# Performance work log

Hardware: AMD Instinct MI355X
Metric: run time of the kernel (lower is better)

The kernel has to match this reference:

```python
import jax, jax.numpy as jnp
import numpy as np
from jax import lax

B = 16384
N_NUM = 32
N_CAT = 16
D = 256
D_HID = 512
N_LAYERS = 8
VOCAB = 100001  # total_cats + 1
OUT_DIM = 2
TOT_FEAT = N_NUM + N_CAT
EPS = 1e-5


def _layernorm(x, g, b):
    mu = jnp.mean(x, axis=-1, keepdims=True)
    var = jnp.mean(jnp.square(x - mu), axis=-1, keepdims=True)
    return (x - mu) * lax.rsqrt(var + EPS) * g + b


def setup_inputs() -> dict:
    key = jax.random.key(0)
    ks = jax.random.split(key, 16)
    s = 0.02
    return {
        "x_numerical": jax.random.normal(ks[0], (B, N_NUM, 1), dtype=jnp.float32),
        "x_categorical_idx": jax.random.randint(ks[1], (B, N_CAT), 0, VOCAB - 1, dtype=jnp.int32),
        # per-feature Linear(1, D): weight [N_NUM, D], bias [N_NUM, D]
        "w_num": jax.random.normal(ks[2], (N_NUM, D), dtype=jnp.float32) * s,
        "b_num": jnp.zeros((N_NUM, D), dtype=jnp.float32),
        "cat_embed": jax.random.normal(ks[3], (VOCAB, D), dtype=jnp.float32) * s,
        "W_first": jax.random.normal(ks[4], (TOT_FEAT * D, D), dtype=jnp.float32) * s,
        "b_first": jnp.zeros((D,), dtype=jnp.float32),
        # stacked block params, leading dim = N_LAYERS
        "ln_g": jnp.ones((N_LAYERS, D), dtype=jnp.float32),
        "ln_b": jnp.zeros((N_LAYERS, D), dtype=jnp.float32),
        "W1s": jax.random.normal(ks[5], (N_LAYERS, D, D_HID), dtype=jnp.float32) * s,
        "b1s": jnp.zeros((N_LAYERS, D_HID), dtype=jnp.float32),
        "W2s": jax.random.normal(ks[6], (N_LAYERS, D_HID, D), dtype=jnp.float32) * s,
        "b2s": jnp.zeros((N_LAYERS, D), dtype=jnp.float32),
        "g_f": jnp.ones((D,), dtype=jnp.float32),
        "beta_f": jnp.zeros((D,), dtype=jnp.float32),
        "W_head": jax.random.normal(ks[7], (D, OUT_DIM), dtype=jnp.float32) * s,
        "b_head": jnp.zeros((OUT_DIM,), dtype=jnp.float32),
    }


def reference(x_numerical, x_categorical_idx, w_num, b_num, cat_embed,
              W_first, b_first, ln_g, ln_b, W1s, b1s, W2s, b2s,
              g_f, beta_f, W_head, b_head):
    # numerical embeddings: per-feature Linear(1, D), vectorized over features
    x_val = x_numerical[:, :, 0:1]                       # [B, N_NUM, 1]
    x_n_emb = x_val * w_num[None] + b_num[None]          # [B, N_NUM, D]
    x_c_emb = cat_embed[x_categorical_idx]               # [B, N_CAT, D]
    x = jnp.concatenate([x_n_emb, x_c_emb], axis=1)      # [B, TOT_FEAT, D]
    x = x.reshape(x.shape[0], -1)                        # [B, TOT_FEAT*D]
    x = x @ W_first + b_first                            # [B, D]

    def block(h, params):
        g, bn, W1, b1, W2, b2 = params
        out = _layernorm(h, g, bn)
        out = jax.nn.relu(out @ W1 + b1)                 # dropout = identity (eval)
        out = out @ W2 + b2
        return h + out, None

    x, _ = lax.scan(block, x, (ln_g, ln_b, W1s, b1s, W2s, b2s))
    x = _layernorm(x, g_f, beta_f)
    logits = x @ W_head + b_head                         # [B, OUT_DIM]
    return logits
```

## Files before the change

### kernel.cpp

```cpp
#include <hip/hip_runtime.h>

typedef unsigned short u16;
typedef unsigned int u32;
typedef __attribute__((ext_vector_type(8))) short bf16x8;
typedef __attribute__((ext_vector_type(4))) float f32x4;

#define LDK 72

__device__ __forceinline__ u16 f2bf(float f) {
    u32 u = __float_as_uint(f);
    u += 0x7fffu + ((u >> 16) & 1u);
    return (u16)(u >> 16);
}

__device__ __forceinline__ f32x4 mfma16(bf16x8 a, bf16x8 b, f32x4 c) {
    return __builtin_amdgcn_mfma_f32_16x16x32_bf16(a, b, c, 0, 0, 0);
}


__global__ __launch_bounds__(256) void prep_u_kernel(
    const float* __restrict__ w_num, const float* __restrict__ b_num,
    const float* __restrict__ W_first, float* __restrict__ Upart, float* __restrict__ Ppart)
{
    __shared__ float wrow[32];
    __shared__ float brow[32];
    int j = threadIdx.x, f = blockIdx.x, ks = blockIdx.y;
    if (j < 32) {
        wrow[j] = w_num[f * 256 + ks * 32 + j];
        brow[j] = b_num[f * 256 + ks * 32 + j];
    }
    __syncthreads();
    float au = 0.f, ap = 0.f;
#pragma unroll 8
    for (int k = 0; k < 32; k++) {
        float w = W_first[(size_t)((f << 8) + ks * 32 + k) * 256 + j];
        au = fmaf(wrow[k], w, au);
        ap = fmaf(brow[k], w, ap);
    }
    Upart[(size_t)(ks * 32 + f) * 256 + j] = au;
    Ppart[(size_t)(ks * 32 + f) * 256 + j] = ap;
}

__global__ __launch_bounds__(256) void prep_reduce_kernel(
    const float* __restrict__ Upart, const float* __restrict__ Ppart,
    float* __restrict__ U, float* __restrict__ P)
{
    int j = threadIdx.x, f = blockIdx.x;
    float au = 0.f, ap = 0.f;
#pragma unroll
    for (int ks = 0; ks < 8; ks++) {
        au += Upart[(size_t)(ks * 32 + f) * 256 + j];
        ap += Ppart[(size_t)(ks * 32 + f) * 256 + j];
    }
    U[f * 256 + j] = au;
    P[f * 256 + j] = ap;
}

__global__ __launch_bounds__(256) void prep_c0_kernel(
    const float* __restrict__ b_first, const float* __restrict__ P, float* __restrict__ c0)
{
    int j = threadIdx.x;
    float a = b_first[j];
#pragma unroll 8
    for (int f = 0; f < 32; f++) a += P[f * 256 + j];
    c0[j] = a;
}

__global__ __launch_bounds__(256) void transpose_kernel(
    const float* __restrict__ in, u16* __restrict__ out,
    int R, int C, int ldo, int k_off, size_t in_stride, size_t out_stride)
{
    __shared__ float t[64][65];
    in  += (size_t)blockIdx.z * in_stride;
    out += (size_t)blockIdx.z * out_stride;
    const int tid = threadIdx.x;
    const int r0 = blockIdx.x * 64, c0 = blockIdx.y * 64;
#pragma unroll
    for (int i = 0; i < 16; i++) {
        int e = tid + i * 256;
        int r = e >> 6, c = e & 63;
        float v = (r0 + r < R) ? in[(size_t)(r0 + r) * C + c0 + c] : 0.f;
        t[c][r] = v;
    }
    __syncthreads();
#pragma unroll
    for (int i = 0; i < 2; i++) {
        int e = tid + i * 256;
        int c = e >> 3, r8 = (e & 7) * 8;
        u16 tmp[8];
#pragma unroll
        for (int x = 0; x < 8; x++) tmp[x] = f2bf(t[c][r8 + x]);
        *(bf16x8*)&out[(size_t)(c0 + c) * ldo + k_off + r0 + r8] = *(bf16x8*)tmp;
    }
}

#define FBM 64

#define GATHER(KQ, G0, G1)                                                    \
    {                                                                         \
        int chunk = tid;                                                      \
        int r = chunk >> 4, c4 = chunk & 15;                                  \
        int k = (KQ) + c4 * 4;                                                \
        int rowi = (k < 4096) ? sidx[r * 16 + ((k >> 8) & 15)] : 0;           \
        G0 = *(const float4*)&cemb[(size_t)rowi * 256 + (k & 255)];           \
        if (k >= 4096) {                                                      \
            if (k < 4128) {                                                   \
                int c = r * 32 + (k - 4096);                                  \
                G0.x = sx[c]; G0.y = sx[c + 1];                               \
                G0.z = sx[c + 2]; G0.w = sx[c + 3];                           \
            } else G0 = make_float4(0.f, 0.f, 0.f, 0.f);                      \
        }                                                                     \
        chunk = tid + 512;                                                    \
        r = chunk >> 4; c4 = chunk & 15;                                      \
        k = (KQ) + c4 * 4;                                                    \
        rowi = (k < 4096) ? sidx[r * 16 + ((k >> 8) & 15)] : 0;               \
        G1 = *(const float4*)&cemb[(size_t)rowi * 256 + (k & 255)];           \
        if (k >= 4096) {                                                      \
            if (k < 4128) {                                                   \
                int c = r * 32 + (k - 4096);                                  \
                G1.x = sx[c]; G1.y = sx[c + 1];                               \
                G1.z = sx[c + 2]; G1.w = sx[c + 3];                           \
            } else G1 = make_float4(0.f, 0.f, 0.f, 0.f);                      \
        }                                                                     \
    }

#define WRITE_A(BUF, G0, G1)                                                  \
    {                                                                         \
        int chunk = tid;                                                      \
        int r = chunk >> 4, c4 = chunk & 15;                                  \
        ushort4 o;                                                            \
        o.x = f2bf(G0.x); o.y = f2bf(G0.y); o.z = f2bf(G0.z); o.w = f2bf(G0.w); \
        *(ushort4*)&Ab[BUF][r * LDK + c4 * 4] = o;                            \
        chunk = tid + 512;                                                    \
        r = chunk >> 4; c4 = chunk & 15;                                      \
        o.x = f2bf(G1.x); o.y = f2bf(G1.y); o.z = f2bf(G1.z); o.w = f2bf(G1.w); \
        *(ushort4*)&Ab[BUF][r * LDK + c4 * 4] = o;                            \
    }

#define DMA_B(BUF, KQ)                                                        \
    _Pragma("unroll")                                                         \
    for (int it = 0; it < 4; it++) {                                          \
        int chunk = it * 512 + tid;                                           \
        int r = chunk >> 3;                                                   \
        int c8 = (chunk & 7) ^ (r & 7);                                       \
        const u16* src = &BT[(size_t)r * 4160 + (KQ) + c8 * 8];               \
        __builtin_amdgcn_global_load_lds(                                     \
            (const __attribute__((address_space(1))) void*)src,               \
            (__attribute__((address_space(3))) void*)&Bb[BUF][(it * 512 + wv * 64) * 8], \
            16, 0, 0);                                                        \
    }

#define COMPUTE(AB, BB)                                                       \
    _Pragma("unroll")                                                         \
    for (int kk = 0; kk < 64; kk += 32) {                                     \
        bf16x8 af[2], bfr[4];                                                 \
        _Pragma("unroll")                                                     \
        for (int i = 0; i < 2; i++)                                           \
            af[i] = *(const bf16x8*)&Ab[AB][(wm * 32 + i * 16 + l16) * LDK + kk + quad * 8]; \
        _Pragma("unroll")                                                     \
        for (int j = 0; j < 4; j++) {                                         \
            int row = wn * 64 + j * 16 + l16;                                 \
            int c8L = quad + (kk >> 3);                                       \
            bfr[j] = *(const bf16x8*)&Bb[BB][row * 64 + ((c8L ^ (row & 7)) * 8)]; \
        }                                                                     \
        _Pragma("unroll")                                                     \
        for (int i = 0; i < 2; i++)                                           \
            _Pragma("unroll")                                                 \
            for (int j = 0; j < 4; j++)                                       \
                acc[i][j] = mfma16(af[i], bfr[j], acc[i][j]);                 \
    }

#define ITER(S, KQ, G0, G1)                                                   \
    {                                                                         \
        WRITE_A((S + 1) & 1, G0, G1);                                         \
        int kq2 = (KQ) + 128; if (kq2 > 4096) kq2 = 4096;                     \
        DMA_B((S + 2) & 3, kq2);                                              \
        __builtin_amdgcn_sched_barrier(0);                                    \
        GATHER((KQ) + 192, G0, G1);                                           \
        __builtin_amdgcn_sched_barrier(0);                                    \
        COMPUTE(S & 1, S);                                                    \
        asm volatile("s_waitcnt vmcnt(8) lgkmcnt(0)" ::: "memory");           \
        __builtin_amdgcn_s_barrier();                                         \
        __builtin_amdgcn_sched_barrier(0);                                    \
    }

__global__ __launch_bounds__(512, 2) void first_gemm_kernel(
    const u16* __restrict__ BT, const float* __restrict__ bias,
    float* __restrict__ outF,
    const int* __restrict__ cidx, const float* __restrict__ cemb,
    const float* __restrict__ xnum)
{
    __shared__ __align__(16) u16 Ab[2][FBM * LDK];
    __shared__ __align__(16) u16 Bb[4][256 * 64];
    __shared__ int   sidx[FBM * 16];
    __shared__ float sx[FBM * 32];

    const int tid  = threadIdx.x;
    const int lane = tid & 63;
    const int wv   = tid >> 6;
    const int wm   = wv >> 2;
    const int wn   = wv & 3;
    const int quad = lane >> 4;
    const int l16  = lane & 15;
    const int m0   = blockIdx.x * FBM;

    sidx[tid]       = cidx[m0 * 16 + tid];
    sidx[tid + 512] = cidx[m0 * 16 + tid + 512];
    {
        float4 v = *(const float4*)&xnum[(size_t)m0 * 32 + tid * 4];
        *(float4*)&sx[tid * 4] = v;
    }
    __syncthreads();

    f32x4 acc[2][4];
#pragma unroll
    for (int i = 0; i < 2; i++)
#pragma unroll
        for (int j = 0; j < 4; j++) acc[i][j] = (f32x4){0.f, 0.f, 0.f, 0.f};

    float4 ga0, ga1, pa0, pa1, pb0, pb1;

    GATHER(0, ga0, ga1);
    WRITE_A(0, ga0, ga1);
    DMA_B(0, 0);
    __builtin_amdgcn_sched_barrier(0);
    GATHER(64, pa0, pa1);
    __builtin_amdgcn_sched_barrier(0);
    DMA_B(1, 64);
    __builtin_amdgcn_sched_barrier(0);
    GATHER(128, pb0, pb1);
    __builtin_amdgcn_sched_barrier(0);
    asm volatile("s_waitcnt vmcnt(8) lgkmcnt(0)" ::: "memory");
    __builtin_amdgcn_s_barrier();
    __builtin_amdgcn_sched_barrier(0);

#pragma unroll 1
    for (int k0 = 0; k0 < 4096; k0 += 256) {
        ITER(0, k0 +   0, pa0, pa1);
        ITER(1, k0 +  64, pb0, pb1);
        ITER(2, k0 + 128, pa0, pa1);
        ITER(3, k0 + 192, pb0, pb1);
    }
    COMPUTE(0, 0);

#pragma unroll
    for (int i = 0; i < 2; i++) {
#pragma unroll
        for (int j = 0; j < 4; j++) {
            int col = wn * 64 + j * 16 + l16;
            float bs = bias[col];
#pragma unroll
            for (int r = 0; r < 4; r++) {
                int row = m0 + wm * 32 + i * 16 + quad * 4 + r;
                outF[(size_t)row * 256 + col] = acc[i][j][r] + bs;
            }
        }
    }
}

#define BAR()                                                                 \
    asm volatile("s_waitcnt lgkmcnt(0)" ::: "memory");                        \
    __builtin_amdgcn_s_barrier();                                             \
    __builtin_amdgcn_sched_barrier(0);

__global__ __launch_bounds__(512, 2) void stack_kernel(
    const float* __restrict__ h,
    const float* __restrict__ ln_g, const float* __restrict__ ln_b,
    const u16* __restrict__ W1T, const float* __restrict__ b1s,
    const u16* __restrict__ W2T, const float* __restrict__ b2s,
    const float* __restrict__ g_f, const float* __restrict__ beta_f,
    const float* __restrict__ Wh, const float* __restrict__ bh,
    float* __restrict__ out)
{
    __shared__ __align__(16) float hbuf[64 * 260];
    __shared__ __align__(16) u16   scratch[64 * 512];
    const int tid  = threadIdx.x;
    const int lane = tid & 63;
    const int wv   = tid >> 6;
    const int quad = lane >> 4;
    const int l16  = lane & 15;
    const int m0   = blockIdx.x * 64;

#pragma unroll
    for (int rr = 0; rr < 8; rr++) {
        int row = rr * 8 + wv;
        *(float4*)&hbuf[row * 260 + lane * 4] =
            *(const float4*)&h[(size_t)(m0 + row) * 256 + lane * 4];
    }
    BAR();

#pragma unroll 1
    for (int l = 0; l < 8; l++) {
        const u16* W1 = W1T + l * 131072;
        const u16* W2 = W2T + l * 131072;
        const float* bb1 = b1s + l * 512;
        const float* bb2 = b2s + l * 256;

        float4 gv4 = *(const float4*)&ln_g[l * 256 + lane * 4];
        float4 bv4 = *(const float4*)&ln_b[l * 256 + lane * 4];
#pragma unroll
        for (int rr = 0; rr < 8; rr++) {
            int row = rr * 8 + wv;
            float4 x = *(const float4*)&hbuf[row * 260 + lane * 4];
            float s  = x.x + x.y + x.z + x.w;
            float s2 = x.x * x.x + x.y * x.y + x.z * x.z + x.w * x.w;
#pragma unroll
            for (int o = 32; o > 0; o >>= 1) { s += __shfl_xor(s, o); s2 += __shfl_xor(s2, o); }
            float mu = s * (1.f / 256.f);
            float rs = rsqrtf(s2 * (1.f / 256.f) - mu * mu + 1e-5f);
            ushort4 o4;
            o4.x = f2bf((x.x - mu) * rs * gv4.x + bv4.x);
            o4.y = f2bf((x.y - mu) * rs * gv4.y + bv4.y);
            o4.z = f2bf((x.z - mu) * rs * gv4.z + bv4.z);
            o4.w = f2bf((x.w - mu) * rs * gv4.w + bv4.w);
            *(ushort4*)&scratch[row * 256 + (((lane >> 1) ^ (row & 7)) << 3) + (lane & 1) * 4] = o4;
        }
        BAR();

        float b1v[4];
#pragma unroll
        for (int j = 0; j < 4; j++) b1v[j] = bb1[wv * 64 + j * 16 + l16];
        f32x4 acc1[4][4];
#pragma unroll
        for (int i = 0; i < 4; i++)
#pragma unroll
            for (int j = 0; j < 4; j++) acc1[i][j] = (f32x4){0.f, 0.f, 0.f, 0.f};
#pragma unroll
        for (int ks = 0; ks < 8; ks++) {
            bf16x8 af[4], bw[4];
#pragma unroll
            for (int i = 0; i < 4; i++)
                af[i] = *(const bf16x8*)&scratch[(i * 16 + l16) * 256 +
                            (((ks * 4 + quad) ^ (l16 & 7)) << 3)];
#pragma unroll
            for (int j = 0; j < 4; j++)
                bw[j] = *(const bf16x8*)&W1[(size_t)(wv * 64 + j * 16 + l16) * 256 + ks * 32 + quad * 8];
#pragma unroll
            for (int i = 0; i < 4; i++)
#pragma unroll
                for (int j = 0; j < 4; j++)
                    acc1[i][j] = mfma16(af[i], bw[j], acc1[i][j]);
        }
        BAR();

#pragma unroll
        for (int i = 0; i < 4; i++)
#pragma unroll
            for (int j = 0; j < 4; j++)
#pragma unroll
                for (int r = 0; r < 4; r++) {
                    float v = acc1[i][j][r] + b1v[j];
                    v = v > 0.f ? v : 0.f;
                    int row2 = i * 16 + quad * 4 + r;
                    int col  = wv * 64 + j * 16 + l16;
                    scratch[row2 * 512 + (((col >> 3) ^ (row2 & 7)) << 3) + (col & 7)] = f2bf(v);
                }
        BAR();

        float b2v[2];
#pragma unroll
        for (int j = 0; j < 2; j++) b2v[j] = bb2[wv * 32 + j * 16 + l16];
        f32x4 acc2[4][2];
#pragma unroll
        for (int i = 0; i < 4; i++)
#pragma unroll
            for (int j = 0; j < 2; j++) acc2[i][j] = (f32x4){0.f, 0.f, 0.f, 0.f};
#pragma unroll
        for (int ks = 0; ks < 16; ks++) {
            bf16x8 af[4], bw[2];
#pragma unroll
            for (int i = 0; i < 4; i++)
                af[i] = *(const bf16x8*)&scratch[(i * 16 + l16) * 512 +
                            (((ks * 4 + quad) ^ (l16 & 7)) << 3)];
#pragma unroll
            for (int j = 0; j < 2; j++)
                bw[j] = *(const bf16x8*)&W2[(size_t)(wv * 32 + j * 16 + l16) * 512 + ks * 32 + quad * 8];
#pragma unroll
            for (int i = 0; i < 4; i++)
#pragma unroll
                for (int j = 0; j < 2; j++)
                    acc2[i][j] = mfma16(af[i], bw[j], acc2[i][j]);
        }

#pragma unroll
        for (int i = 0; i < 4; i++)
#pragma unroll
            for (int j = 0; j < 2; j++) {
                int col = wv * 32 + j * 16 + l16;
#pragma unroll
                for (int r = 0; r < 4; r++)
                    hbuf[(i * 16 + quad * 4 + r) * 260 + col] += acc2[i][j][r] + b2v[j];
            }
        BAR();
    }

    {
        float4 gv4 = *(const float4*)&g_f[lane * 4];
        float4 bv4 = *(const float4*)&beta_f[lane * 4];
        float4 wa = *(const float4*)&Wh[lane * 8];
        float4 wb = *(const float4*)&Wh[lane * 8 + 4];
        float bh0 = bh[0], bh1 = bh[1];
#pragma unroll
        for (int rr = 0; rr < 8; rr++) {
            int row = rr * 8 + wv;
            float4 x = *(const float4*)&hbuf[row * 260 + lane * 4];
            float s = x.x + x.y + x.z + x.w;
            float s2 = x.x * x.x + x.y * x.y + x.z * x.z + x.w * x.w;
#pragma unroll
            for (int o = 32; o > 0; o >>= 1) { s += __shfl_xor(s, o); s2 += __shfl_xor(s2, o); }
            float mu = s * (1.f / 256.f);
            float rs = rsqrtf(s2 * (1.f / 256.f) - mu * mu + 1e-5f);
            float xn0 = (x.x - mu) * rs * gv4.x + bv4.x;
            float xn1 = (x.y - mu) * rs * gv4.y + bv4.y;
            float xn2 = (x.z - mu) * rs * gv4.z + bv4.z;
            float xn3 = (x.w - mu) * rs * gv4.w + bv4.w;
            float d0 = xn0 * wa.x + xn1 * wa.z + xn2 * wb.x + xn3 * wb.z;
            float d1 = xn0 * wa.y + xn1 * wa.w + xn2 * wb.y + xn3 * wb.w;
#pragma unroll
            for (int o = 32; o > 0; o >>= 1) { d0 += __shfl_xor(d0, o); d1 += __shfl_xor(d1, o); }
            if (lane == 0) {
                out[(size_t)(m0 + row) * 2 + 0] = d0 + bh0;
                out[(size_t)(m0 + row) * 2 + 1] = d1 + bh1;
            }
        }
    }
}

extern "C" void kernel_launch(void* const* d_in, const int* in_sizes, int n_in,
                              void* d_out, int out_size, void* d_ws, size_t ws_size,
                              hipStream_t stream)
{
    const float* x_num   = (const float*)d_in[0];
    const int*   cidx    = (const int*)d_in[1];
    const float* w_num   = (const float*)d_in[2];
    const float* b_num   = (const float*)d_in[3];
    const float* cemb    = (const float*)d_in[4];
    const float* W_first = (const float*)d_in[5];
    const float* b_first = (const float*)d_in[6];
    const float* ln_g    = (const float*)d_in[7];
    const float* ln_b    = (const float*)d_in[8];
    const float* W1s     = (const float*)d_in[9];
    const float* b1s     = (const float*)d_in[10];
    const float* W2s     = (const float*)d_in[11];
    const float* b2s     = (const float*)d_in[12];
    const float* g_f     = (const float*)d_in[13];
    const float* beta_f  = (const float*)d_in[14];
    const float* W_head  = (const float*)d_in[15];
    const float* b_head  = (const float*)d_in[16];
    float* out = (float*)d_out;

    char* ws = (char*)d_ws;
    float* U   = (float*)(ws + 0);
    float* c0  = (float*)(ws + 32768);
    float* P   = (float*)(ws + 33792);
    u16* WcT   = (u16*)(ws + 66560);
    u16* W1T   = (u16*)(ws + 2196480);
    u16* W2T   = (u16*)(ws + 4293632);
    float* h   = (float*)(ws + 6390784);
    float* Upart = (float*)(ws + 2196480);
    float* Ppart = (float*)(ws + 2458624);

    prep_u_kernel<<<dim3(32, 8), 256, 0, stream>>>(w_num, b_num, W_first, Upart, Ppart);
    prep_reduce_kernel<<<32, 256, 0, stream>>>(Upart, Ppart, U, P);
    prep_c0_kernel<<<1, 256, 0, stream>>>(b_first, P, c0);
    transpose_kernel<<<dim3(64, 4, 1), 256, 0, stream>>>(
        W_first + (size_t)8192 * 256, WcT, 4096, 256, 4160, 0, 0, 0);
    transpose_kernel<<<dim3(1, 4, 1), 256, 0, stream>>>(
        U, WcT, 32, 256, 4160, 4096, 0, 0);
    transpose_kernel<<<dim3(4, 8, 8), 256, 0, stream>>>(
        W1s, W1T, 256, 512, 256, 0, 131072, 131072);
    transpose_kernel<<<dim3(8, 4, 8), 256, 0, stream>>>(
        W2s, W2T, 512, 256, 512, 0, 131072, 131072);

    first_gemm_kernel<<<256, 512, 0, stream>>>(
        WcT, c0, h, cidx, cemb, x_num);

    stack_kernel<<<256, 512, 0, stream>>>(
        h, ln_g, ln_b, W1T, b1s, W2T, b2s,
        g_f, beta_f, W_head, b_head, out);
}
```

Measured before the change: 463.7 us.

## Retile residual stack to 32-row blocks and fold bias reduction into first GEMM

The MLP stack kernel now processes 32 rows per block with 4 waves (512 blocks of 256 threads) instead of 64 rows with 8 waves. Each wave now covers more output columns, and LDS uses padded strides in place of the XOR swizzle. The separate c0 bias-reduction kernel is removed, and its sum over P is computed inside the first GEMM epilogue. This is meant to raise block count and parallelism and to drop one launch. The cost is that each weight tile is reused across half as many rows, so global weight traffic per row doubles, and padded LDS may bring bank conflicts.

```diff
diff --git a/kernel.cpp b/kernel.cpp
--- a/kernel.cpp
+++ b/kernel.cpp
@@ -54,16 +54,6 @@
     }
     U[f * 256 + j] = au;
     P[f * 256 + j] = ap;
-}
-
-__global__ __launch_bounds__(256) void prep_c0_kernel(
-    const float* __restrict__ b_first, const float* __restrict__ P, float* __restrict__ c0)
-{
-    int j = threadIdx.x;
-    float a = b_first[j];
-#pragma unroll 8
-    for (int f = 0; f < 32; f++) a += P[f * 256 + j];
-    c0[j] = a;
 }
 
 __global__ __launch_bounds__(256) void transpose_kernel(
@@ -185,7 +175,8 @@
     }
 
 __global__ __launch_bounds__(512, 2) void first_gemm_kernel(
-    const u16* __restrict__ BT, const float* __restrict__ bias,
+    const u16* __restrict__ BT, const float* __restrict__ bfirst,
+    const float* __restrict__ Pm,
     float* __restrict__ outF,
     const int* __restrict__ cidx, const float* __restrict__ cemb,
     const float* __restrict__ xnum)
@@ -243,27 +234,30 @@
     }
     COMPUTE(0, 0);
 
+    float bsv[4];
+#pragma unroll
+    for (int j = 0; j < 4; j++) {
+        int col = wn * 64 + j * 16 + l16;
+        float bs = bfirst[col];
+#pragma unroll 8
+        for (int f = 0; f < 32; f++) bs += Pm[f * 256 + col];
+        bsv[j] = bs;
+    }
 #pragma unroll
     for (int i = 0; i < 2; i++) {
 #pragma unroll
         for (int j = 0; j < 4; j++) {
             int col = wn * 64 + j * 16 + l16;
-            float bs = bias[col];
 #pragma unroll
             for (int r = 0; r < 4; r++) {
                 int row = m0 + wm * 32 + i * 16 + quad * 4 + r;
-                outF[(size_t)row * 256 + col] = acc[i][j][r] + bs;
+                outF[(size_t)row * 256 + col] = acc[i][j][r] + bsv[j];
             }
         }
     }
 }
 
-#define BAR()                                                                 \
-    asm volatile("s_waitcnt lgkmcnt(0)" ::: "memory");                        \
-    __builtin_amdgcn_s_barrier();                                             \
-    __builtin_amdgcn_sched_barrier(0);
-
-__global__ __launch_bounds__(512, 2) void stack_kernel(
+__global__ __launch_bounds__(256, 2) void stack_kernel(
     const float* __restrict__ h,
     const float* __restrict__ ln_g, const float* __restrict__ ln_b,
     const u16* __restrict__ W1T, const float* __restrict__ b1s,
@@ -272,22 +266,22 @@
     const float* __restrict__ Wh, const float* __restrict__ bh,
     float* __restrict__ out)
 {
-    __shared__ __align__(16) float hbuf[64 * 260];
-    __shared__ __align__(16) u16   scratch[64 * 512];
+    __shared__ __align__(16) float hbuf[32 * 260];
+    __shared__ __align__(16) u16   scratch[32 * 520];
     const int tid  = threadIdx.x;
     const int lane = tid & 63;
     const int wv   = tid >> 6;
     const int quad = lane >> 4;
     const int l16  = lane & 15;
-    const int m0   = blockIdx.x * 64;
+    const int m0   = blockIdx.x * 32;
 
 #pragma unroll
     for (int rr = 0; rr < 8; rr++) {
-        int row = rr * 8 + wv;
+        int row = rr * 4 + wv;
         *(float4*)&hbuf[row * 260 + lane * 4] =
             *(const float4*)&h[(size_t)(m0 + row) * 256 + lane * 4];
     }
-    BAR();
+    __syncthreads();
 
 #pragma unroll 1
     for (int l = 0; l < 8; l++) {
@@ -300,7 +294,7 @@
         float4 bv4 = *(const float4*)&ln_b[l * 256 + lane * 4];
 #pragma unroll
         for (int rr = 0; rr < 8; rr++) {
-            int row = rr * 8 + wv;
+            int row = rr * 4 + wv;
             float4 x = *(const float4*)&hbuf[row * 260 + lane * 4];
             float s  = x.x + x.y + x.z + x.w;
             float s2 = x.x * x.x + x.y * x.y + x.z * x.z + x.w * x.w;
@@ -313,85 +307,81 @@
             o4.y = f2bf((x.y - mu) * rs * gv4.y + bv4.y);
             o4.z = f2bf((x.z - mu) * rs * gv4.z + bv4.z);
             o4.w = f2bf((x.w - mu) * rs * gv4.w + bv4.w);
-            *(ushort4*)&scratch[row * 256 + (((lane >> 1) ^ (row & 7)) << 3) + (lane & 1) * 4] = o4;
+            *(ushort4*)&scratch[row * 264 + lane * 4] = o4;
         }
-        BAR();
-
-        float b1v[4];
-#pragma unroll
-        for (int j = 0; j < 4; j++) b1v[j] = bb1[wv * 64 + j * 16 + l16];
-        f32x4 acc1[4][4];
-#pragma unroll
-        for (int i = 0; i < 4; i++)
-#pragma unroll
-            for (int j = 0; j < 4; j++) acc1[i][j] = (f32x4){0.f, 0.f, 0.f, 0.f};
-#pragma unroll
-        for (int ks = 0; ks < 8; ks++) {
-            bf16x8 af[4], bw[4];
-#pragma unroll
-            for (int i = 0; i < 4; i++)
-                af[i] = *(const bf16x8*)&scratch[(i * 16 + l16) * 256 +
-                            (((ks * 4 + quad) ^ (l16 & 7)) << 3)];
-#pragma unroll
-            for (int j = 0; j < 4; j++)
-                bw[j] = *(const bf16x8*)&W1[(size_t)(wv * 64 + j * 16 + l16) * 256 + ks * 32 + quad * 8];
-#pragma unroll
-            for (int i = 0; i < 4; i++)
-#pragma unroll
-                for (int j = 0; j < 4; j++)
+        __syncthreads();
+
+        float b1v[8];
+#pragma unroll
+        for (int j = 0; j < 8; j++) b1v[j] = bb1[wv * 128 + j * 16 + l16];
+        f32x4 acc1[2][8];
+#pragma unroll
+        for (int i = 0; i < 2; i++)
+#pragma unroll
+            for (int j = 0; j < 8; j++) acc1[i][j] = (f32x4){0.f, 0.f, 0.f, 0.f};
+#pragma unroll
+        for (int kk = 0; kk < 256; kk += 32) {
+            bf16x8 af[2], bw[8];
+#pragma unroll
+            for (int i = 0; i < 2; i++)
+                af[i] = *(const bf16x8*)&scratch[(i * 16 + l16) * 264 + kk + quad * 8];
+#pragma unroll
+            for (int j = 0; j < 8; j++)
+                bw[j] = *(const bf16x8*)&W1[(size_t)(wv * 128 + j * 16 + l16) * 256 + kk + quad * 8];
+#pragma unroll
+            for (int i = 0; i < 2; i++)
+#pragma unroll
+                for (int j = 0; j < 8; j++)
                     acc1[i][j] = mfma16(af[i], bw[j], acc1[i][j]);
         }
-        BAR();
-
-#pragma unroll
-        for (int i = 0; i < 4; i++)
-#pragma unroll
-            for (int j = 0; j < 4; j++)
+        __syncthreads();
+
+#pragma unroll
+        for (int i = 0; i < 2; i++)
+#pragma unroll
+            for (int j = 0; j < 8; j++)
 #pragma unroll
                 for (int r = 0; r < 4; r++) {
                     float v = acc1[i][j][r] + b1v[j];
                     v = v > 0.f ? v : 0.f;
-                    int row2 = i * 16 + quad * 4 + r;
-                    int col  = wv * 64 + j * 16 + l16;
-                    scratch[row2 * 512 + (((col >> 3) ^ (row2 & 7)) << 3) + (col & 7)] = f2bf(v);
+                    scratch[(i * 16 + quad * 4 + r) * 520 + wv * 128 + j * 16 + l16] = f2bf(v);
                 }
-        BAR();
-
-        float b2v[2];
-#pragma unroll
-        for (int j = 0; j < 2; j++) b2v[j] = bb2[wv * 32 + j * 16 + l16];
-        f32x4 acc2[4][2];
-#pragma unroll
-        for (int i = 0; i < 4; i++)
-#pragma unroll
-            for (int j = 0; j < 2; j++) acc2[i][j] = (f32x4){0.f, 0.f, 0.f, 0.f};
-#pragma unroll
-        for (int ks = 0; ks < 16; ks++) {
-            bf16x8 af[4], bw[2];
-#pragma unroll
-            for (int i = 0; i < 4; i++)
-                af[i] = *(const bf16x8*)&scratch[(i * 16 + l16) * 512 +
-                            (((ks * 4 + quad) ^ (l16 & 7)) << 3)];
-#pragma unroll
-            for (int j = 0; j < 2; j++)
-                bw[j] = *(const bf16x8*)&W2[(size_t)(wv * 32 + j * 16 + l16) * 512 + ks * 32 + quad * 8];
-#pragma unroll
-            for (int i = 0; i < 4; i++)
-#pragma unroll
-                for (int j = 0; j < 2; j++)
+        __syncthreads();
+
+        float b2v[4];
+#pragma unroll
+        for (int j = 0; j < 4; j++) b2v[j] = bb2[wv * 64 + j * 16 + l16];
+        f32x4 acc2[2][4];
+#pragma unroll
+        for (int i = 0; i < 2; i++)
+#pragma unroll
+            for (int j = 0; j < 4; j++) acc2[i][j] = (f32x4){0.f, 0.f, 0.f, 0.f};
+#pragma unroll
+        for (int kk = 0; kk < 512; kk += 32) {
+            bf16x8 af[2], bw[4];
+#pragma unroll
+            for (int i = 0; i < 2; i++)
+                af[i] = *(const bf16x8*)&scratch[(i * 16 + l16) * 520 + kk + quad * 8];
+#pragma unroll
+            for (int j = 0; j < 4; j++)
+                bw[j] = *(const bf16x8*)&W2[(size_t)(wv * 64 + j * 16 + l16) * 512 + kk + quad * 8];
+#pragma unroll
+            for (int i = 0; i < 2; i++)
+#pragma unroll
+                for (int j = 0; j < 4; j++)
                     acc2[i][j] = mfma16(af[i], bw[j], acc2[i][j]);
         }
 
 #pragma unroll
-        for (int i = 0; i < 4; i++)
-#pragma unroll
-            for (int j = 0; j < 2; j++) {
-                int col = wv * 32 + j * 16 + l16;
+        for (int i = 0; i < 2; i++)
+#pragma unroll
+            for (int j = 0; j < 4; j++) {
+                int col = wv * 64 + j * 16 + l16;
 #pragma unroll
                 for (int r = 0; r < 4; r++)
                     hbuf[(i * 16 + quad * 4 + r) * 260 + col] += acc2[i][j][r] + b2v[j];
             }
-        BAR();
+        __syncthreads();
     }
 
     {
@@ -402,7 +392,7 @@
         float bh0 = bh[0], bh1 = bh[1];
 #pragma unroll
         for (int rr = 0; rr < 8; rr++) {
-            int row = rr * 8 + wv;
+            int row = rr * 4 + wv;
             float4 x = *(const float4*)&hbuf[row * 260 + lane * 4];
             float s = x.x + x.y + x.z + x.w;
             float s2 = x.x * x.x + x.y * x.y + x.z * x.z + x.w * x.w;
@@ -451,7 +441,6 @@
 
     char* ws = (char*)d_ws;
     float* U   = (float*)(ws + 0);
-    float* c0  = (float*)(ws + 32768);
     float* P   = (float*)(ws + 33792);
     u16* WcT   = (u16*)(ws + 66560);
     u16* W1T   = (u16*)(ws + 2196480);
@@ -462,7 +451,6 @@
 
     prep_u_kernel<<<dim3(32, 8), 256, 0, stream>>>(w_num, b_num, W_first, Upart, Ppart);
     prep_reduce_kernel<<<32, 256, 0, stream>>>(Upart, Ppart, U, P);
-    prep_c0_kernel<<<1, 256, 0, stream>>>(b_first, P, c0);
     transpose_kernel<<<dim3(64, 4, 1), 256, 0, stream>>>(
         W_first + (size_t)8192 * 256, WcT, 4096, 256, 4160, 0, 0, 0);
     transpose_kernel<<<dim3(1, 4, 1), 256, 0, stream>>>(
@@ -473,9 +461,9 @@
         W2s, W2T, 512, 256, 512, 0, 131072, 131072);
 
     first_gemm_kernel<<<256, 512, 0, stream>>>(
-        WcT, c0, h, cidx, cemb, x_num);
-
-    stack_kernel<<<256, 512, 0, stream>>>(
+        WcT, b_first, P, h, cidx, cemb, x_num);
+
+    stack_kernel<<<512, 256, 0, stream>>>(
         h, ln_g, ln_b, W1T, b1s, W2T, b2s,
         g_f, beta_f, W_head, b_head, out);
 }
```

After: 602.0 us. 1.3x slower.
